# Kernel tuning notes

Hardware: AMD Instinct MI355X
Metric: run time of the kernel (lower is better)

## Reference

```python
import jax, jax.numpy as jnp
import numpy as np

HEIGHT = 8  # init kwarg: output crop height
B, J, C, HIMG, WIMG = 8, 64, 32, 256, 256


def _make_boxes():
    rng = np.random.default_rng(0)
    left = rng.uniform(0.0, 40.0, (B, J))
    bw = rng.uniform(16.0, 200.0, (B, J))
    top = rng.uniform(0.0, 200.0, (B, J))
    bh = rng.uniform(8.0, 32.0, (B, J))
    theta = rng.uniform(-0.5, 0.5, (B, J))  # unused by the original forward
    return np.stack([left, top, left + bw, top + bh, theta], axis=-1).astype(np.float32)


def _box_widths(boxes_np):
    # torch: width = int(aspect * height), truncation (values are positive)
    bw = boxes_np[..., 2] - boxes_np[..., 0]
    bh = boxes_np[..., 3] - boxes_np[..., 1]
    return ((bw / bh) * HEIGHT).astype(np.int32)  # [B, J]


def setup_inputs() -> dict:
    key = jax.random.key(0)
    image = jax.random.normal(key, (B, C, HIMG, WIMG), dtype=jnp.float32)
    boxes = jnp.asarray(_make_boxes())
    return {"image": image, "boxes": boxes}


def reference(image, boxes):
    # Per-box widths are integer (shape-determining) constants, taken from concrete box data.
    boxes_np = np.asarray(jax.device_get(boxes))
    widths_np = _box_widths(boxes_np)          # [B, J] ints >= 2
    max_w = int(widths_np.max())
    widths = jnp.asarray(widths_np)

    dt = boxes.dtype
    base_w = boxes[..., 2] - boxes[..., 0]      # [B, J]
    base_h = boxes[..., 3] - boxes[..., 1]
    each_w = base_w / (widths.astype(dt) - 1)   # [B, J]
    each_h = base_h / (HEIGHT - 1)

    # Sampling grids: xx [B,J,Wm], yy [B,J,Hh]
    xx = jnp.arange(max_w, dtype=dt)[None, None, :] * each_w[..., None] + boxes[..., 0:1]
    yy = jnp.arange(HEIGHT, dtype=dt)[None, None, :] * each_h[..., None] + boxes[..., 1:2]

    def interp_one_image(img, x, y):
        # img [C,Hi,Wi], x [J,Wm], y [J,Hh] -> [C,J,Hh,Wm]
        x0 = jnp.clip(jnp.floor(x).astype(jnp.int32), 0, WIMG - 1)
        x1 = jnp.clip(jnp.floor(x).astype(jnp.int32) + 1, 0, WIMG - 1)
        y0 = jnp.clip(jnp.floor(y).astype(jnp.int32), 0, HIMG - 1)
        y1 = jnp.clip(jnp.floor(y).astype(jnp.int32) + 1, 0, HIMG - 1)
        # gathers: [C, J, Hh, Wm]
        ia = img[:, y0[:, :, None], x0[:, None, :]]
        ib = img[:, y1[:, :, None], x0[:, None, :]]
        ic = img[:, y0[:, :, None], x1[:, None, :]]
        idd = img[:, y1[:, :, None], x1[:, None, :]]
        x0f, x1f = x0.astype(dt), x1.astype(dt)
        y0f, y1f = y0.astype(dt), y1.astype(dt)
        wa = (x1f - x)[:, None, :] * (y1f - y)[:, :, None]  # [J,Hh,Wm]
        wb = (x1f - x)[:, None, :] * (y - y0f)[:, :, None]
        wc = (x - x0f)[:, None, :] * (y1f - y)[:, :, None]
        wd = (x - x0f)[:, None, :] * (y - y0f)[:, :, None]
        return ia * wa[None] + ib * wb[None] + ic * wc[None] + idd * wd[None]

    res = jax.vmap(interp_one_image)(image, xx, yy)      # [B,C,J,Hh,Wm]
    res = jnp.transpose(res, (0, 2, 1, 3, 4))            # [B,J,C,Hh,Wm]

    mask = (jnp.arange(max_w)[None, None, :] < widths[..., None]).astype(jnp.uint8)  # [B,J,Wm]
    res = res * mask[:, :, None, None, :].astype(res.dtype)  # zero-pad beyond each box width
    return res, mask
```

## Files before the change

kernel.cpp:

```cpp
#include <hip/hip_runtime.h>

#define HIMG 256
#define WIMG 256
#define CCH  32
#define JBOX 64
#define BIMG 8
#define HGT  8
#define CPB  8
#define NCG  (CCH / CPB)

__global__ __launch_bounds__(256, 8) void roi_kernel(
    const float* __restrict__ img,
    const float* __restrict__ boxes,
    float* __restrict__ res,
    float* __restrict__ mask,
    int max_w)
{
    const int d    = blockIdx.x;
    const int slot = d & 7;
    const int seq  = d >> 3;
    const int bj   = slot * ((BIMG * JBOX) / 8) + (seq >> 2);
    const int cg   = seq & 3;
    const int b    = bj >> 6;
    const int tid  = threadIdx.x;

    const float left = boxes[bj * 5 + 0];
    const float top  = boxes[bj * 5 + 1];
    const float bw   = boxes[bj * 5 + 2] - left;
    const float bh   = boxes[bj * 5 + 3] - top;

    const int   width  = (int)(bw / bh * 8.0f);
    const float each_w = bw / ((float)width - 1.0f);
    const float each_h = bh / 7.0f;

    const int  i = tid;
    if (i >= max_w) return;
    const bool in_w = (i < width);

    if (cg == 0) {
        mask[(size_t)bj * max_w + i] = in_w ? 1.0f : 0.0f;
    }

    const float x  = __fadd_rn(__fmul_rn((float)i, each_w), left);
    const int   xf = (int)floorf(x);
    const int   x0 = min(max(xf, 0), WIMG - 1);
    const float wx1 = (float)(x0 + 1) - x;
    const float wx0 = x - (float)x0;
    const int   lx  = min(x0, WIMG - 2);

    const float* base = img + ((size_t)b * CCH + cg * CPB) * (HIMG * WIMG) + lx;
    float* resp0 = res + (((size_t)bj * CCH + cg * CPB) * HGT) * (size_t)max_w + i;

    #pragma unroll
    for (int h = 0; h < HGT; ++h) {
        const float yh  = __fadd_rn(__fmul_rn((float)h, each_h), top);
        const int   yfl = (int)floorf(yh);
        const int   ya  = min(max(yfl,     0), HIMG - 1);
        const int   yb  = min(max(yfl + 1, 0), HIMG - 1);
        const float wy1 = (float)yb - yh;
        const float wy0 = yh - (float)ya;

        const float wa  = wx1 * wy1;
        const float wb_ = wx1 * wy0;
        const float wc_ = wx0 * wy1;
        const float wd_ = wx0 * wy0;

        const float* r0p = base + (size_t)ya * WIMG;
        const float* r1p = base + (size_t)yb * WIMG;
        float* resph = resp0 + (size_t)h * max_w;

        #pragma unroll
        for (int c = 0; c < CPB; ++c) {
            const float* p0 = r0p + (size_t)c * (HIMG * WIMG);
            const float* p1 = r1p + (size_t)c * (HIMG * WIMG);
            const float v00 = p0[0];
            const float v01 = p0[1];
            const float v10 = p1[0];
            const float v11 = p1[1];
            const float val = v00 * wa + v10 * wb_ + v01 * wc_ + v11 * wd_;
            __builtin_nontemporal_store(in_w ? val : 0.0f,
                                        resph + (size_t)c * (HGT * (size_t)max_w));
        }
    }
}

extern "C" void kernel_launch(void* const* d_in, const int* in_sizes, int n_in,
                              void* d_out, int out_size, void* d_ws, size_t ws_size,
                              hipStream_t stream) {
    const float* img   = (const float*)d_in[0];
    const float* boxes = (const float*)d_in[1];
    float* out = (float*)d_out;

    const int per_w = BIMG * JBOX * CCH * HGT + BIMG * JBOX;
    const int max_w = out_size / per_w;

    float* res  = out;
    float* mask = out + (size_t)BIMG * JBOX * CCH * HGT * max_w;

    const int blocks = BIMG * JBOX * NCG;
    roi_kernel<<<blocks, 256, 0, stream>>>(img, boxes, res, mask, max_w);
}
```

Before: 167.0 us.

## Stage full image rows into LDS with async global_load_lds triple buffering per wave

Each wave now handles one channel of one box. For every output row it copies the two source image rows (the full 256-float width) into LDS using async global-to-LDS loads, triple-buffered with manual vmcnt waits. The bilinear taps are then read from LDS instead of from scattered global loads, and the block-to-work mapping is changed to interleave images. This swaps a small number of gathered global reads for full-row streaming, which may fetch more bytes than needed for narrow boxes, and it adds LDS pressure and lowers the occupancy hint.

```diff
diff --git a/kernel.cpp b/kernel.cpp
--- a/kernel.cpp
+++ b/kernel.cpp
@@ -6,23 +6,29 @@
 #define JBOX 64
 #define BIMG 8
 #define HGT  8
-#define CPB  8
-#define NCG  (CCH / CPB)
+#define NBUF 3
 
-__global__ __launch_bounds__(256, 8) void roi_kernel(
+typedef __attribute__((address_space(3))) float lds_f;
+typedef const __attribute__((address_space(1))) float glb_f;
+
+__global__ __launch_bounds__(256, 6) void roi_kernel(
     const float* __restrict__ img,
     const float* __restrict__ boxes,
     float* __restrict__ res,
     float* __restrict__ mask,
     int max_w)
 {
+    __shared__ float sbuf[4][NBUF][2][WIMG];
+
     const int d    = blockIdx.x;
-    const int slot = d & 7;
-    const int seq  = d >> 3;
-    const int bj   = slot * ((BIMG * JBOX) / 8) + (seq >> 2);
-    const int cg   = seq & 3;
-    const int b    = bj >> 6;
+    const int b    = d & 7;
+    const int q    = d >> 3;
     const int tid  = threadIdx.x;
+    const int wv   = tid >> 6;
+    const int lane = tid & 63;
+    const int c    = (q & 7) * 4 + wv;
+    const int j    = q >> 3;
+    const int bj   = b * JBOX + j;
 
     const float left = boxes[bj * 5 + 0];
     const float top  = boxes[bj * 5 + 1];
@@ -33,53 +39,106 @@
     const float each_w = bw / ((float)width - 1.0f);
     const float each_h = bh / 7.0f;
 
-    const int  i = tid;
-    if (i >= max_w) return;
-    const bool in_w = (i < width);
-
-    if (cg == 0) {
-        mask[(size_t)bj * max_w + i] = in_w ? 1.0f : 0.0f;
+    int   lxk[4];
+    float wx0k[4], wx1k[4];
+    #pragma unroll
+    for (int k = 0; k < 4; ++k) {
+        const int   i  = 64 * k + lane;
+        const float x  = __fadd_rn(__fmul_rn((float)i, each_w), left);
+        const int   xf = (int)floorf(x);
+        const int   x0 = min(max(xf, 0), WIMG - 1);
+        wx1k[k] = (float)(x0 + 1) - x;
+        wx0k[k] = x - (float)x0;
+        lxk[k]  = min(x0, WIMG - 2);
     }
 
-    const float x  = __fadd_rn(__fmul_rn((float)i, each_w), left);
-    const int   xf = (int)floorf(x);
-    const int   x0 = min(max(xf, 0), WIMG - 1);
-    const float wx1 = (float)(x0 + 1) - x;
-    const float wx0 = x - (float)x0;
-    const int   lx  = min(x0, WIMG - 2);
+    const float* chbase = img + (size_t)(b * CCH + c) * (HIMG * WIMG);
 
-    const float* base = img + ((size_t)b * CCH + cg * CPB) * (HIMG * WIMG) + lx;
-    float* resp0 = res + (((size_t)bj * CCH + cg * CPB) * HGT) * (size_t)max_w + i;
+    auto dma = [&](int h, int bf) {
+        const float yh  = __fadd_rn(__fmul_rn((float)h, each_h), top);
+        const int   yfl = (int)floorf(yh);
+        const int   ya  = min(max(yfl,     0), HIMG - 1);
+        const int   yb  = min(max(yfl + 1, 0), HIMG - 1);
+        const float* s0 = chbase + (size_t)ya * WIMG + 4 * lane;
+        const float* s1 = chbase + (size_t)yb * WIMG + 4 * lane;
+        __builtin_amdgcn_global_load_lds((glb_f*)s0, (lds_f*)&sbuf[wv][bf][0][0], 16, 0, 0);
+        __builtin_amdgcn_global_load_lds((glb_f*)s1, (lds_f*)&sbuf[wv][bf][1][0], 16, 0, 0);
+    };
 
-    #pragma unroll
-    for (int h = 0; h < HGT; ++h) {
+    auto consume = [&](int h, int bf, float4& A) {
         const float yh  = __fadd_rn(__fmul_rn((float)h, each_h), top);
         const int   yfl = (int)floorf(yh);
         const int   ya  = min(max(yfl,     0), HIMG - 1);
         const int   yb  = min(max(yfl + 1, 0), HIMG - 1);
         const float wy1 = (float)yb - yh;
         const float wy0 = yh - (float)ya;
+        float vals[4];
+        #pragma unroll
+        for (int k = 0; k < 4; ++k) {
+            const float v00 = sbuf[wv][bf][0][lxk[k]];
+            const float v01 = sbuf[wv][bf][0][lxk[k] + 1];
+            const float v10 = sbuf[wv][bf][1][lxk[k]];
+            const float v11 = sbuf[wv][bf][1][lxk[k] + 1];
+            const float wa  = wx1k[k] * wy1;
+            const float wb_ = wx1k[k] * wy0;
+            const float wc_ = wx0k[k] * wy1;
+            const float wd_ = wx0k[k] * wy0;
+            vals[k] = v00 * wa + v10 * wb_ + v01 * wc_ + v11 * wd_;
+        }
+        A.x = vals[0]; A.y = vals[1]; A.z = vals[2]; A.w = vals[3];
+    };
 
-        const float wa  = wx1 * wy1;
-        const float wb_ = wx1 * wy0;
-        const float wc_ = wx0 * wy1;
-        const float wd_ = wx0 * wy0;
+    float4 a0, a1, a2, a3, a4, a5, a6, a7;
 
-        const float* r0p = base + (size_t)ya * WIMG;
-        const float* r1p = base + (size_t)yb * WIMG;
-        float* resph = resp0 + (size_t)h * max_w;
+    dma(0, 0);
+    dma(1, 1);
+    dma(2, 2);
+    __builtin_amdgcn_sched_barrier(0);
 
+#define STEP(H, BF, WN, A)                                                    \
+    do {                                                                      \
+        asm volatile("s_waitcnt vmcnt(" #WN ")" ::: "memory");                \
+        __builtin_amdgcn_sched_barrier(0);                                    \
+        consume(H, BF, A);                                                    \
+                \
+        asm volatile("s_waitcnt lgkmcnt(0)" ::: "memory");                    \
+        __builtin_amdgcn_sched_barrier(0);                                    \
+        if ((H) + 3 < HGT) dma((H) + 3, BF);                                  \
+    } while (0)
+
+    STEP(0, 0, 4, a0);
+    STEP(1, 1, 4, a1);
+    STEP(2, 2, 4, a2);
+    STEP(3, 0, 4, a3);
+    STEP(4, 1, 4, a4);
+    STEP(5, 2, 4, a5);
+    STEP(6, 0, 2, a6);
+    STEP(7, 1, 0, a7);
+#undef STEP
+
+    float* rb = res + ((size_t)(bj * CCH + c) * HGT) * (size_t)max_w;
+
+#define STORE_H(H, A)                                                         \
+    do {                                                                      \
+        const float vals[4] = {A.x, A.y, A.z, A.w};                           \
+        _Pragma("unroll")                                                     \
+        for (int k = 0; k < 4; ++k) {                                         \
+            const int ii = 64 * k + lane;                                     \
+            if (ii < max_w)                                                   \
+                rb[(size_t)(H) * max_w + ii] = (ii < width) ? vals[k] : 0.0f; \
+        }                                                                     \
+    } while (0)
+
+    STORE_H(0, a0); STORE_H(1, a1); STORE_H(2, a2); STORE_H(3, a3);
+    STORE_H(4, a4); STORE_H(5, a5); STORE_H(6, a6); STORE_H(7, a7);
+#undef STORE_H
+
+    if (c == 0) {
         #pragma unroll
-        for (int c = 0; c < CPB; ++c) {
-            const float* p0 = r0p + (size_t)c * (HIMG * WIMG);
-            const float* p1 = r1p + (size_t)c * (HIMG * WIMG);
-            const float v00 = p0[0];
-            const float v01 = p0[1];
-            const float v10 = p1[0];
-            const float v11 = p1[1];
-            const float val = v00 * wa + v10 * wb_ + v01 * wc_ + v11 * wd_;
-            __builtin_nontemporal_store(in_w ? val : 0.0f,
-                                        resph + (size_t)c * (HGT * (size_t)max_w));
+        for (int k = 0; k < 4; ++k) {
+            const int ii = 64 * k + lane;
+            if (ii < max_w)
+                mask[(size_t)bj * max_w + ii] = (ii < width) ? 1.0f : 0.0f;
         }
     }
 }
@@ -97,6 +156,6 @@
     float* res  = out;
     float* mask = out + (size_t)BIMG * JBOX * CCH * HGT * max_w;
 
-    const int blocks = BIMG * JBOX * NCG;
+    const int blocks = BIMG * JBOX * CCH / 4;
     roi_kernel<<<blocks, 256, 0, stream>>>(img, boxes, res, mask, max_w);
 }
```

After: 286.6 us. 71.7% more time.
